# Kernel optimization log

Measured on AMD Instinct MI355X. Metric: run time of the kernel, lower is better.

The kernel has to match this reference:

```python
import jax, jax.numpy as jnp
import numpy as np

INTERP = 10  # gt contour interpolation factor (time=10 in source)
SMOOTH_L1_BETA = 1.0
LOSS_WEIGHT = 1.0


def interpolation(poly):
    # poly: [B, M, 2] -> [B, M*INTERP, 2]
    poly_roll = jnp.roll(poly, shift=1, axis=1)
    step = jnp.arange(INTERP, dtype=poly.dtype) / INTERP  # [INTERP]
    # [B, M, INTERP, 2]
    interp = (poly[:, :, None, :] * step[None, None, :, None]
              + poly_roll[:, :, None, :] * (1.0 - step)[None, None, :, None])
    B, M = poly.shape[0], poly.shape[1]
    return interp.reshape(B, M * INTERP, 2)


def compute_distance(pred, gt):
    # pred: [B, N, 2], gt: [B, M, 2] -> squared euclidean distance [B, M, N]
    # ||g - p||^2 = ||g||^2 + ||p||^2 - 2 g.p  (avoids materializing [B,M,N,2])
    g2 = jnp.sum(gt * gt, axis=-1)[:, :, None]    # [B, M, 1]
    p2 = jnp.sum(pred * pred, axis=-1)[:, None, :]  # [B, 1, N]
    gp = jnp.einsum('bmk,bnk->bmn', gt, pred)
    return g2 + p2 - 2.0 * gp


def smooth_l1(x, y):
    d = jnp.abs(x - y)
    return jnp.where(d < SMOOTH_L1_BETA, 0.5 * d * d / SMOOTH_L1_BETA, d - 0.5 * SMOOTH_L1_BETA)


def setup_inputs() -> dict:
    key = jax.random.key(0)
    k1, k2, k3, k4 = jax.random.split(key, 4)
    B, N, M = 1024, 128, 128
    ini_pred_poly = jax.random.normal(k1, (B, N, 2), dtype=jnp.float32)
    pred_poly = ini_pred_poly + 0.1 * jax.random.normal(k2, (B, N, 2), dtype=jnp.float32)
    gt_poly = jax.random.normal(k3, (B, M, 2), dtype=jnp.float32)
    keyPointsMask = (jax.random.uniform(k4, (B, M)) < 0.7).astype(jnp.float32)
    return {'ini_pred_poly': ini_pred_poly, 'pred_poly': pred_poly,
            'gt_poly': gt_poly, 'keyPointsMask': keyPointsMask}


def reference(ini_pred_poly, pred_poly, gt_poly, keyPointsMask):
    # --- lossPred2NearestGt ---
    gt_interp = interpolation(gt_poly)                       # [B, M*10, 2]
    d1 = compute_distance(ini_pred_poly, gt_interp)          # [B, M*10, N]
    index_gt = jnp.argmin(d1, axis=1)                        # [B, N]
    nearest_gt = jnp.take_along_axis(gt_interp, index_gt[:, :, None], axis=1)  # [B, N, 2]
    loss_pred2gt = jnp.mean(smooth_l1(pred_poly, nearest_gt))  # scalar (reduction='mean')

    # --- lossGt2NearestPred ---
    d2 = compute_distance(ini_pred_poly, gt_poly)            # [B, M, N]
    index_pred = jnp.argmin(d2, axis=2)                      # [B, M]
    nearest_pred = jnp.take_along_axis(pred_poly, index_pred[:, :, None], axis=1)  # [B, M, 2]
    loss_gt2pred = smooth_l1(nearest_pred, gt_poly)          # [B, M, 2] (reduction='none')

    # mask expanded to [B, M, 2] in the source -> its sum counts both coords
    mask = keyPointsMask[:, :, None]
    masked_sum = jnp.sum(loss_gt2pred * mask)
    mask_sum = 2.0 * jnp.sum(keyPointsMask)
    loss_set2set = masked_sum / (mask_sum + 1.0) + loss_pred2gt
    loss = loss_set2set / 2.0
    return LOSS_WEIGHT * loss
```

## Files before the change

### kernel.cpp

```cpp
#include <hip/hip_runtime.h>
#include <math.h>


#define BB 1024
#define NN 128
#define MM 128

__device__ __forceinline__ float sl1(float x) {
    float d = fabsf(x);
    return d < 1.0f ? 0.5f * d * d : d - 0.5f;
}

__global__ void __launch_bounds__(256, 8)
dmloss_main(const float* __restrict__ ini, const float* __restrict__ pred,
            const float* __restrict__ gt,  const float* __restrict__ kmask,
            float4* __restrict__ partials)
{
    const int b    = blockIdx.x >> 1;
    const int half = blockIdx.x & 1;
    const int tid  = threadIdx.x;
    const int g    = tid & 63;
    const int h    = tid >> 6;
    const int P    = (half << 6) + g;

    __shared__ __align__(16) float2 s_gt[MM];
    __shared__ float2 s_pr[NN];
    __shared__ float2 s_ii[NN];
    __shared__ float4 s_seg[MM];
    __shared__ float  s_step[16];
    __shared__ float  s_rv[4 * 64];
    __shared__ float  s_rf[4 * 64];
    __shared__ float  s_sum[3][4];

    const float2* gt2 = (const float2*)(gt   + (size_t)b * MM * 2);
    const float2* in2 = (const float2*)(ini  + (size_t)b * NN * 2);
    const float2* pr2 = (const float2*)(pred + (size_t)b * NN * 2);

    if (tid < 128) {
        int m = tid;
        float2 gm = gt2[m];
        float2 a  = gt2[(m + 127) & 127];
        s_gt[m] = gm;
        float ex = gm.x - a.x, ey = gm.y - a.y;
        float A  = ex * ex + ey * ey;
        float inv5 = A > 0.f ? 5.f / A : 0.f;
        s_seg[m] = make_float4(gm.x, gm.y, inv5, A * 0.01f);
        if (tid < 16) s_step[tid] = (float)tid / 10.0f;
    } else {
        int k = tid - 128;
        s_pr[k] = pr2[k];
        s_ii[k] = in2[k];
    }
    float2 myP  = in2[P];
    float2 myG  = gt2[P];
    const float px = myP.x, py = myP.y;
    __syncthreads();

    float sumA = 0.f, sumB = 0.f, sumC = 0.f;

    float b0 = INFINITY, f0 = 1e30f;
    {
        const int m0 = 32 * h;
        float2 a0 = s_gt[(m0 + 127) & 127];
        float dax = a0.x - px, day = a0.y - py;
        float Da = fmaf(day, day, dax * dax);
        float fm = (float)(320 * h);
        #pragma unroll 4
        for (int j = 0; j < 32; ++j) {
            float4 S = s_seg[m0 + j];
            float dgx = S.x - px, dgy = S.y - py;
            float Dg  = fmaf(dgy, dgy, dgx * dgx);
            float jv  = fmaf(Da - Dg, S.z, 5.0f);
            float jr  = rintf(__builtin_amdgcn_fmed3f(jv, 0.f, 9.f));
            float t   = fmaf(jv, -2.f, jr);
            float d   = fmaf(S.w * jr, t, Da);
            float fi  = fm + jr;
            if (d < b0) { b0 = d; f0 = fi; }
            Da = Dg;
            fm += 10.f;
        }
    }
    s_rv[h * 64 + g] = b0;
    s_rf[h * 64 + g] = f0;
    __syncthreads();

    if (tid < 64) {
        float best = s_rv[tid], bf = s_rf[tid];
        #pragma unroll
        for (int q = 1; q < 4; ++q) {
            float ov = s_rv[q * 64 + tid];
            float of = s_rf[q * 64 + tid];
            if (ov < best || (ov == best && of < bf)) { best = ov; bf = of; }
        }
        int bidx = (int)bf;
        int m = bidx / 10;
        int j = bidx - m * 10;
        float s  = s_step[j];
        float tt = 1.0f - s;
        float2 gm = s_gt[m];
        float2 gp = s_gt[(m + 127) & 127];
        float gx = gm.x * s + gp.x * tt;
        float gy = gm.y * s + gp.y * tt;
        float2 pr = s_pr[(half << 6) + tid];
        sumA = sl1(pr.x - gx) + sl1(pr.y - gy);
    }
    __syncthreads();

    {
        const float gx = myG.x, gy = myG.y;
        float b1 = INFINITY, f1 = 1e30f;
        float fk = (float)(32 * h);
        const int k0 = 32 * h;
        #pragma unroll 4
        for (int j = 0; j < 32; ++j) {
            float2 I = s_ii[k0 + j];
            float dx = I.x - gx, dy = I.y - gy;
            float d  = fmaf(dy, dy, dx * dx);
            if (d < b1) { b1 = d; f1 = fk; }
            fk += 1.f;
        }
        s_rv[h * 64 + g] = b1;
        s_rf[h * 64 + g] = f1;
    }
    __syncthreads();

    if (tid < 64) {
        float best = s_rv[tid], bf = s_rf[tid];
        #pragma unroll
        for (int q = 1; q < 4; ++q) {
            float ov = s_rv[q * 64 + tid];
            float of = s_rf[q * 64 + tid];
            if (ov < best || (ov == best && of < bf)) { best = ov; bf = of; }
        }
        int k = (int)bf;
        float2 pk2 = s_pr[k];
        float2 g0  = s_gt[(half << 6) + tid];
        float  km  = kmask[b * MM + (half << 6) + tid];
        sumB = km * (sl1(pk2.x - g0.x) + sl1(pk2.y - g0.y));
        sumC = km;
    }

    #pragma unroll
    for (int off = 32; off > 0; off >>= 1) {
        sumA += __shfl_down(sumA, off);
        sumB += __shfl_down(sumB, off);
        sumC += __shfl_down(sumC, off);
    }
    const int wave = tid >> 6;
    if ((tid & 63) == 0) {
        s_sum[0][wave] = sumA; s_sum[1][wave] = sumB; s_sum[2][wave] = sumC;
    }
    __syncthreads();
    if (tid == 0) {
        float A = 0.f, Bs = 0.f, C = 0.f;
        #pragma unroll
        for (int w = 0; w < 4; ++w) {
            A += s_sum[0][w]; Bs += s_sum[1][w]; C += s_sum[2][w];
        }
        partials[blockIdx.x] = make_float4(A, Bs, C, 0.0f);
    }
}

__global__ void __launch_bounds__(256)
dmloss_final(const float4* __restrict__ partials, float* __restrict__ out)
{
    const int tid = threadIdx.x;
    float A = 0.0f, Bs = 0.0f, C = 0.0f;
    #pragma unroll
    for (int i = tid; i < 2 * BB; i += 256) {
        float4 p = partials[i];
        A += p.x; Bs += p.y; C += p.z;
    }
    #pragma unroll
    for (int off = 32; off > 0; off >>= 1) {
        A  += __shfl_down(A, off);
        Bs += __shfl_down(Bs, off);
        C  += __shfl_down(C, off);
    }
    __shared__ float sA[4], sB[4], sC[4];
    const int wave = tid >> 6, lane = tid & 63;
    if (lane == 0) { sA[wave] = A; sB[wave] = Bs; sC[wave] = C; }
    __syncthreads();
    if (tid == 0) {
        float a  = sA[0] + sA[1] + sA[2] + sA[3];
        float bs = sB[0] + sB[1] + sB[2] + sB[3];
        float c  = sC[0] + sC[1] + sC[2] + sC[3];
        float loss_pred2gt = a / ((float)BB * (float)NN * 2.0f);
        float loss_set2set = bs / (2.0f * c + 1.0f) + loss_pred2gt;
        out[0] = 0.5f * loss_set2set;
    }
}

extern "C" void kernel_launch(void* const* d_in, const int* in_sizes, int n_in,
                              void* d_out, int out_size, void* d_ws, size_t ws_size,
                              hipStream_t stream)
{
    const float* ini   = (const float*)d_in[0];
    const float* pred  = (const float*)d_in[1];
    const float* gt    = (const float*)d_in[2];
    const float* kmask = (const float*)d_in[3];
    float4* partials = (float4*)d_ws;

    dmloss_main<<<dim3(2 * BB), dim3(256), 0, stream>>>(ini, pred, gt, kmask, partials);
    dmloss_final<<<dim3(1), dim3(256), 0, stream>>>(partials, (float*)d_out);
}
```

Measured before the change: 17.86 us.

## Split argmin phases into separate blocks and reduce via packed u64 shuffles

The two nearest-neighbour searches now run in separate blocks. A grid of 3*B blocks gives 2*B blocks to pred→gt and B blocks to gt→pred. Within each block, the partial argmins from the 4 (or 2) threads sharing a point are combined with shuffle-xor on packed (distance bits, index) 64-bit keys. This replaces the shared-memory staging and extra barriers. The change is meant to remove the serial phase dependence and the LDS round trips, at the cost of more blocks, redundant input loads, and 64-bit compares and shuffles.

```diff
diff --git a/kernel.cpp b/kernel.cpp
--- a/kernel.cpp
+++ b/kernel.cpp
@@ -6,6 +6,9 @@
 #define NN 128
 #define MM 128
 
+typedef unsigned long long u64;
+typedef unsigned int u32;
+
 __device__ __forceinline__ float sl1(float x) {
     float d = fabsf(x);
     return d < 1.0f ? 0.5f * d * d : d - 0.5f;
@@ -14,162 +17,156 @@
 __global__ void __launch_bounds__(256, 8)
 dmloss_main(const float* __restrict__ ini, const float* __restrict__ pred,
             const float* __restrict__ gt,  const float* __restrict__ kmask,
-            float4* __restrict__ partials)
+            float* __restrict__ pA, float2* __restrict__ pBC)
 {
-    const int b    = blockIdx.x >> 1;
-    const int half = blockIdx.x & 1;
-    const int tid  = threadIdx.x;
-    const int g    = tid & 63;
-    const int h    = tid >> 6;
-    const int P    = (half << 6) + g;
-
-    __shared__ __align__(16) float2 s_gt[MM];
-    __shared__ float2 s_pr[NN];
-    __shared__ float2 s_ii[NN];
+    const int bid = blockIdx.x;
+    const int tid = threadIdx.x;
+
     __shared__ float4 s_seg[MM];
     __shared__ float  s_step[16];
-    __shared__ float  s_rv[4 * 64];
-    __shared__ float  s_rf[4 * 64];
-    __shared__ float  s_sum[3][4];
-
-    const float2* gt2 = (const float2*)(gt   + (size_t)b * MM * 2);
-    const float2* in2 = (const float2*)(ini  + (size_t)b * NN * 2);
-    const float2* pr2 = (const float2*)(pred + (size_t)b * NN * 2);
-
-    if (tid < 128) {
-        int m = tid;
-        float2 gm = gt2[m];
-        float2 a  = gt2[(m + 127) & 127];
-        s_gt[m] = gm;
-        float ex = gm.x - a.x, ey = gm.y - a.y;
-        float A  = ex * ex + ey * ey;
-        float inv5 = A > 0.f ? 5.f / A : 0.f;
-        s_seg[m] = make_float4(gm.x, gm.y, inv5, A * 0.01f);
-        if (tid < 16) s_step[tid] = (float)tid / 10.0f;
+    __shared__ float2 s_ii[NN];
+    __shared__ float2 s_pr[NN];
+    __shared__ float  s_sum[2][4];
+    const int wave = tid >> 6;
+
+    if (bid < 2 * BB) {
+        const int b    = bid >> 1;
+        const int half = bid & 1;
+        const int q    = tid & 3;
+        const int P    = (half << 6) + (tid >> 2);
+
+        const float2* gt2 = (const float2*)(gt  + (size_t)b * MM * 2);
+        const float2* in2 = (const float2*)(ini + (size_t)b * NN * 2);
+        const float2* pr2 = (const float2*)(pred + (size_t)b * NN * 2);
+
+        if (tid < 128) {
+            int m = tid;
+            float2 gm = gt2[m];
+            float2 a  = gt2[(m + 127) & 127];
+            float ex = gm.x - a.x, ey = gm.y - a.y;
+            float A  = ex * ex + ey * ey;
+            float inv5 = A > 0.f ? 5.f / A : 0.f;
+            s_seg[m] = make_float4(gm.x, gm.y, inv5, A * 0.01f);
+            if (tid < 16) s_step[tid] = (float)tid / 10.0f;
+        }
+        float2 myP  = in2[P];
+        float2 myPr = make_float2(0.f, 0.f);
+        if (q == 0) myPr = pr2[P];
+        const float px = myP.x, py = myP.y;
+        __syncthreads();
+
+        u64 best = ~0ull;
+        {
+            const int m0 = 32 * q;
+            float2 a0 = make_float2(s_seg[(m0 + 127) & 127].x,
+                                    s_seg[(m0 + 127) & 127].y);
+            float dax = a0.x - px, day = a0.y - py;
+            float Da = fmaf(day, day, dax * dax);
+            int bi = 10 * m0;
+            #pragma unroll 4
+            for (int j = 0; j < 32; ++j) {
+                float4 S = s_seg[m0 + j];
+                float dgx = S.x - px, dgy = S.y - py;
+                float Dg  = fmaf(dgy, dgy, dgx * dgx);
+                float jv  = fmaf(Da - Dg, S.z, 5.0f);
+                float jr  = rintf(__builtin_amdgcn_fmed3f(jv, 0.f, 9.f));
+                float t   = fmaf(jv, -2.f, jr);
+                float d   = fmaf(S.w * jr, t, Da);
+                u64 c = ((u64)__builtin_bit_cast(u32, d) << 32)
+                        | (u32)(bi + (int)jr);
+                if (c < best) best = c;
+                Da = Dg;
+                bi += 10;
+            }
+        }
+        { u64 o = __shfl_xor(best, 1); if (o < best) best = o; }
+        { u64 o = __shfl_xor(best, 2); if (o < best) best = o; }
+
+        float sumA = 0.f;
+        if (q == 0) {
+            u32 idx = (u32)best;
+            int m = (int)idx / 10;
+            int j = (int)idx - 10 * m;
+            float s  = s_step[j];
+            float tt = 1.0f - s;
+            float4 Sm = s_seg[m];
+            float4 Sp = s_seg[(m + 127) & 127];
+            float gx = Sm.x * s + Sp.x * tt;
+            float gy = Sm.y * s + Sp.y * tt;
+            sumA = sl1(myPr.x - gx) + sl1(myPr.y - gy);
+        }
+        #pragma unroll
+        for (int off = 32; off > 0; off >>= 1) sumA += __shfl_down(sumA, off);
+        if ((tid & 63) == 0) s_sum[0][wave] = sumA;
+        __syncthreads();
+        if (tid == 0)
+            pA[bid] = s_sum[0][0] + s_sum[0][1] + s_sum[0][2] + s_sum[0][3];
     } else {
-        int k = tid - 128;
-        s_pr[k] = pr2[k];
-        s_ii[k] = in2[k];
-    }
-    float2 myP  = in2[P];
-    float2 myG  = gt2[P];
-    const float px = myP.x, py = myP.y;
-    __syncthreads();
-
-    float sumA = 0.f, sumB = 0.f, sumC = 0.f;
-
-    float b0 = INFINITY, f0 = 1e30f;
-    {
-        const int m0 = 32 * h;
-        float2 a0 = s_gt[(m0 + 127) & 127];
-        float dax = a0.x - px, day = a0.y - py;
-        float Da = fmaf(day, day, dax * dax);
-        float fm = (float)(320 * h);
-        #pragma unroll 4
-        for (int j = 0; j < 32; ++j) {
-            float4 S = s_seg[m0 + j];
-            float dgx = S.x - px, dgy = S.y - py;
-            float Dg  = fmaf(dgy, dgy, dgx * dgx);
-            float jv  = fmaf(Da - Dg, S.z, 5.0f);
-            float jr  = rintf(__builtin_amdgcn_fmed3f(jv, 0.f, 9.f));
-            float t   = fmaf(jv, -2.f, jr);
-            float d   = fmaf(S.w * jr, t, Da);
-            float fi  = fm + jr;
-            if (d < b0) { b0 = d; f0 = fi; }
-            Da = Dg;
-            fm += 10.f;
-        }
-    }
-    s_rv[h * 64 + g] = b0;
-    s_rf[h * 64 + g] = f0;
-    __syncthreads();
-
-    if (tid < 64) {
-        float best = s_rv[tid], bf = s_rf[tid];
+        const int b = bid - 2 * BB;
+        const int q = tid & 1;
+        const int m = tid >> 1;
+
+        const float2* gt2 = (const float2*)(gt  + (size_t)b * MM * 2);
+        const float2* in2 = (const float2*)(ini + (size_t)b * NN * 2);
+        const float2* pr2 = (const float2*)(pred + (size_t)b * NN * 2);
+
+        if (tid < 128) {
+            s_ii[tid] = in2[tid];
+            s_pr[tid] = pr2[tid];
+        }
+        float2 myG = gt2[m];
+        float  myKm = 0.f;
+        if (q == 0) myKm = kmask[b * MM + m];
+        const float gx = myG.x, gy = myG.y;
+        __syncthreads();
+
+        u64 best = ~0ull;
+        {
+            const int k0 = 64 * q;
+            #pragma unroll 4
+            for (int j = 0; j < 64; ++j) {
+                float2 I = s_ii[k0 + j];
+                float dx = I.x - gx, dy = I.y - gy;
+                float d  = fmaf(dy, dy, dx * dx);
+                u64 c = ((u64)__builtin_bit_cast(u32, d) << 32)
+                        | (u32)(k0 + j);
+                if (c < best) best = c;
+            }
+        }
+        { u64 o = __shfl_xor(best, 1); if (o < best) best = o; }
+
+        float sumB = 0.f, sumC = 0.f;
+        if (q == 0) {
+            u32 k = (u32)best;
+            float2 pk = s_pr[k];
+            sumB = myKm * (sl1(pk.x - gx) + sl1(pk.y - gy));
+            sumC = myKm;
+        }
         #pragma unroll
-        for (int q = 1; q < 4; ++q) {
-            float ov = s_rv[q * 64 + tid];
-            float of = s_rf[q * 64 + tid];
-            if (ov < best || (ov == best && of < bf)) { best = ov; bf = of; }
-        }
-        int bidx = (int)bf;
-        int m = bidx / 10;
-        int j = bidx - m * 10;
-        float s  = s_step[j];
-        float tt = 1.0f - s;
-        float2 gm = s_gt[m];
-        float2 gp = s_gt[(m + 127) & 127];
-        float gx = gm.x * s + gp.x * tt;
-        float gy = gm.y * s + gp.y * tt;
-        float2 pr = s_pr[(half << 6) + tid];
-        sumA = sl1(pr.x - gx) + sl1(pr.y - gy);
-    }
-    __syncthreads();
-
-    {
-        const float gx = myG.x, gy = myG.y;
-        float b1 = INFINITY, f1 = 1e30f;
-        float fk = (float)(32 * h);
-        const int k0 = 32 * h;
-        #pragma unroll 4
-        for (int j = 0; j < 32; ++j) {
-            float2 I = s_ii[k0 + j];
-            float dx = I.x - gx, dy = I.y - gy;
-            float d  = fmaf(dy, dy, dx * dx);
-            if (d < b1) { b1 = d; f1 = fk; }
-            fk += 1.f;
-        }
-        s_rv[h * 64 + g] = b1;
-        s_rf[h * 64 + g] = f1;
-    }
-    __syncthreads();
-
-    if (tid < 64) {
-        float best = s_rv[tid], bf = s_rf[tid];
-        #pragma unroll
-        for (int q = 1; q < 4; ++q) {
-            float ov = s_rv[q * 64 + tid];
-            float of = s_rf[q * 64 + tid];
-            if (ov < best || (ov == best && of < bf)) { best = ov; bf = of; }
-        }
-        int k = (int)bf;
-        float2 pk2 = s_pr[k];
-        float2 g0  = s_gt[(half << 6) + tid];
-        float  km  = kmask[b * MM + (half << 6) + tid];
-        sumB = km * (sl1(pk2.x - g0.x) + sl1(pk2.y - g0.y));
-        sumC = km;
-    }
-
-    #pragma unroll
-    for (int off = 32; off > 0; off >>= 1) {
-        sumA += __shfl_down(sumA, off);
-        sumB += __shfl_down(sumB, off);
-        sumC += __shfl_down(sumC, off);
-    }
-    const int wave = tid >> 6;
-    if ((tid & 63) == 0) {
-        s_sum[0][wave] = sumA; s_sum[1][wave] = sumB; s_sum[2][wave] = sumC;
-    }
-    __syncthreads();
-    if (tid == 0) {
-        float A = 0.f, Bs = 0.f, C = 0.f;
-        #pragma unroll
-        for (int w = 0; w < 4; ++w) {
-            A += s_sum[0][w]; Bs += s_sum[1][w]; C += s_sum[2][w];
-        }
-        partials[blockIdx.x] = make_float4(A, Bs, C, 0.0f);
+        for (int off = 32; off > 0; off >>= 1) {
+            sumB += __shfl_down(sumB, off);
+            sumC += __shfl_down(sumC, off);
+        }
+        if ((tid & 63) == 0) { s_sum[0][wave] = sumB; s_sum[1][wave] = sumC; }
+        __syncthreads();
+        if (tid == 0)
+            pBC[b] = make_float2(s_sum[0][0] + s_sum[0][1] + s_sum[0][2] + s_sum[0][3],
+                                 s_sum[1][0] + s_sum[1][1] + s_sum[1][2] + s_sum[1][3]);
     }
 }
 
 __global__ void __launch_bounds__(256)
-dmloss_final(const float4* __restrict__ partials, float* __restrict__ out)
+dmloss_final(const float* __restrict__ pA, const float2* __restrict__ pBC,
+             float* __restrict__ out)
 {
     const int tid = threadIdx.x;
     float A = 0.0f, Bs = 0.0f, C = 0.0f;
     #pragma unroll
-    for (int i = tid; i < 2 * BB; i += 256) {
-        float4 p = partials[i];
-        A += p.x; Bs += p.y; C += p.z;
+    for (int i = tid; i < 2 * BB; i += 256) A += pA[i];
+    #pragma unroll
+    for (int i = tid; i < BB; i += 256) {
+        float2 p = pBC[i];
+        Bs += p.x; C += p.y;
     }
     #pragma unroll
     for (int off = 32; off > 0; off >>= 1) {
@@ -199,8 +196,11 @@
     const float* pred  = (const float*)d_in[1];
     const float* gt    = (const float*)d_in[2];
     const float* kmask = (const float*)d_in[3];
-    float4* partials = (float4*)d_ws;
-
-    dmloss_main<<<dim3(2 * BB), dim3(256), 0, stream>>>(ini, pred, gt, kmask, partials);
-    dmloss_final<<<dim3(1), dim3(256), 0, stream>>>(partials, (float*)d_out);
-}
+
+    float*  pA  = (float*)d_ws;
+    float2* pBC = (float2*)(pA + 2 * BB);
+
+    dmloss_main<<<dim3(3 * BB), dim3(256), 0, stream>>>(ini, pred, gt, kmask,
+                                                        pA, pBC);
+    dmloss_final<<<dim3(1), dim3(256), 0, stream>>>(pA, pBC, (float*)d_out);
+}
```

New measurement: 21.79 us. 22.0% more time.

## Precompute segment table in prep kernel and read it via scalar constant loads

Applied to the files above, without the earlier changes.

Adds a prep kernel that computes the per-segment table (point, 5/|e|^2, |e|^2/100) into workspace. The main kernel then reads this table and the ini points through address-space-4 pointers with wave-uniform indices (readfirstlane), so the loads can become scalar loads instead of LDS reads. This removes LDS staging and LDS read traffic from the inner loops. In exchange it adds a third kernel launch and a global write and re-read of 2 MB of segment data, and it relies on the compiler emitting scalar loads.

```diff
diff --git a/kernel.cpp b/kernel.cpp
--- a/kernel.cpp
+++ b/kernel.cpp
@@ -6,15 +6,36 @@
 #define NN 128
 #define MM 128
 
+typedef float f4 __attribute__((ext_vector_type(4)));
+typedef __attribute__((address_space(4))) const f4* c4p;
+
 __device__ __forceinline__ float sl1(float x) {
     float d = fabsf(x);
     return d < 1.0f ? 0.5f * d * d : d - 0.5f;
 }
 
+__global__ void __launch_bounds__(128)
+dmloss_prep(const float* __restrict__ gt, float* __restrict__ seg)
+{
+    const int b = blockIdx.x;
+    const int m = threadIdx.x;
+    __shared__ float2 sg[MM];
+    const float2* g2 = (const float2*)(gt + (size_t)b * MM * 2);
+    sg[m] = g2[m];
+    __syncthreads();
+    float2 g = sg[m];
+    float2 a = sg[(m + 127) & 127];
+    float ex = g.x - a.x, ey = g.y - a.y;
+    float A  = ex * ex + ey * ey;
+    float inv5 = A > 0.f ? 5.f / A : 0.f;
+    float* o = seg + ((size_t)b * MM + m) * 4;
+    o[0] = g.x; o[1] = g.y; o[2] = inv5; o[3] = A * 0.01f;
+}
+
 __global__ void __launch_bounds__(256, 8)
 dmloss_main(const float* __restrict__ ini, const float* __restrict__ pred,
             const float* __restrict__ gt,  const float* __restrict__ kmask,
-            float4* __restrict__ partials)
+            const float* __restrict__ seg, float4* __restrict__ partials)
 {
     const int b    = blockIdx.x >> 1;
     const int half = blockIdx.x & 1;
@@ -22,11 +43,10 @@
     const int g    = tid & 63;
     const int h    = tid >> 6;
     const int P    = (half << 6) + g;
+    const int hs   = __builtin_amdgcn_readfirstlane(h);
 
     __shared__ __align__(16) float2 s_gt[MM];
     __shared__ float2 s_pr[NN];
-    __shared__ float2 s_ii[NN];
-    __shared__ float4 s_seg[MM];
     __shared__ float  s_step[16];
     __shared__ float  s_rv[4 * 64];
     __shared__ float  s_rf[4 * 64];
@@ -37,37 +57,31 @@
     const float2* pr2 = (const float2*)(pred + (size_t)b * NN * 2);
 
     if (tid < 128) {
-        int m = tid;
-        float2 gm = gt2[m];
-        float2 a  = gt2[(m + 127) & 127];
-        s_gt[m] = gm;
-        float ex = gm.x - a.x, ey = gm.y - a.y;
-        float A  = ex * ex + ey * ey;
-        float inv5 = A > 0.f ? 5.f / A : 0.f;
-        s_seg[m] = make_float4(gm.x, gm.y, inv5, A * 0.01f);
+        s_gt[tid] = gt2[tid];
         if (tid < 16) s_step[tid] = (float)tid / 10.0f;
     } else {
-        int k = tid - 128;
-        s_pr[k] = pr2[k];
-        s_ii[k] = in2[k];
-    }
-    float2 myP  = in2[P];
-    float2 myG  = gt2[P];
+        s_pr[tid - 128] = pr2[tid - 128];
+    }
+    float2 myP = in2[P];
+    float2 myG = gt2[P];
     const float px = myP.x, py = myP.y;
+
+    c4p segc = (c4p)(uintptr_t)(seg + (size_t)b * MM * 4);
+    c4p inic = (c4p)(uintptr_t)(ini + (size_t)b * (NN * 2) + 64 * hs);
     __syncthreads();
 
     float sumA = 0.f, sumB = 0.f, sumC = 0.f;
 
     float b0 = INFINITY, f0 = 1e30f;
     {
-        const int m0 = 32 * h;
-        float2 a0 = s_gt[(m0 + 127) & 127];
-        float dax = a0.x - px, day = a0.y - py;
+        const int m0 = 32 * hs;
+        f4 Sp = segc[(m0 + 127) & 127];
+        float dax = Sp.x - px, day = Sp.y - py;
         float Da = fmaf(day, day, dax * dax);
-        float fm = (float)(320 * h);
+        float fm = (float)(320 * hs);
         #pragma unroll 4
         for (int j = 0; j < 32; ++j) {
-            float4 S = s_seg[m0 + j];
+            f4 S = segc[m0 + j];
             float dgx = S.x - px, dgy = S.y - py;
             float Dg  = fmaf(dgy, dgy, dgx * dgx);
             float jv  = fmaf(Da - Dg, S.z, 5.0f);
@@ -109,15 +123,21 @@
     {
         const float gx = myG.x, gy = myG.y;
         float b1 = INFINITY, f1 = 1e30f;
-        float fk = (float)(32 * h);
-        const int k0 = 32 * h;
+        float fk = (float)(32 * hs);
         #pragma unroll 4
-        for (int j = 0; j < 32; ++j) {
-            float2 I = s_ii[k0 + j];
-            float dx = I.x - gx, dy = I.y - gy;
-            float d  = fmaf(dy, dy, dx * dx);
-            if (d < b1) { b1 = d; f1 = fk; }
-            fk += 1.f;
+        for (int j = 0; j < 16; ++j) {
+            f4 I = inic[j];
+            {
+                float dx = I.x - gx, dy = I.y - gy;
+                float d  = fmaf(dy, dy, dx * dx);
+                if (d < b1) { b1 = d; f1 = fk; }
+            }
+            {
+                float dx = I.z - gx, dy = I.w - gy;
+                float d  = fmaf(dy, dy, dx * dx);
+                if (d < b1) { b1 = d; f1 = fk + 1.f; }
+            }
+            fk += 2.f;
         }
         s_rv[h * 64 + g] = b1;
         s_rf[h * 64 + g] = f1;
@@ -199,8 +219,12 @@
     const float* pred  = (const float*)d_in[1];
     const float* gt    = (const float*)d_in[2];
     const float* kmask = (const float*)d_in[3];
-    float4* partials = (float4*)d_ws;
-
-    dmloss_main<<<dim3(2 * BB), dim3(256), 0, stream>>>(ini, pred, gt, kmask, partials);
+
+    float*  seg      = (float*)d_ws;
+    float4* partials = (float4*)(seg + (size_t)BB * MM * 4);
+
+    dmloss_prep<<<dim3(BB), dim3(128), 0, stream>>>(gt, seg);
+    dmloss_main<<<dim3(2 * BB), dim3(256), 0, stream>>>(ini, pred, gt, kmask,
+                                                        seg, partials);
     dmloss_final<<<dim3(1), dim3(256), 0, stream>>>(partials, (float*)d_out);
 }
```

Measured after the change: 24.16 us. 1.35x slower.
